# Kernel tuning notes

Hardware: AMD Instinct MI355X
Metric: run time of the kernel (lower is better)

## Reference

```python
import jax, jax.numpy as jnp
import numpy as np

N_NODES = 50000
N_EDGES = 800000
F_IN = 64
HID = 256
N_GRAPHS = 128
N_OUT = 24


def _sage_conv(x, src, dst, deg_inv, wl, bl, wr):
    # PyG SAGEConv (aggr='mean'): out = lin_l(mean_{j in N(i)} x_j) + lin_r(x_i)
    agg = jax.ops.segment_sum(x[src], dst, num_segments=x.shape[0]) * deg_inv
    return agg @ wl.T + bl + x @ wr.T


def setup_inputs() -> dict:
    key = jax.random.key(0)
    ks = jax.random.split(key, 16)
    x = jax.random.normal(ks[0], (N_NODES, F_IN), dtype=jnp.float32)
    edge_index = jax.random.randint(ks[1], (2, N_EDGES), 0, N_NODES, dtype=jnp.int64)
    batch = jnp.sort(jax.random.randint(ks[2], (N_NODES,), 0, N_GRAPHS, dtype=jnp.int64))

    def lin(k, fan_out, fan_in):
        bound = 1.0 / np.sqrt(fan_in)
        return jax.random.uniform(k, (fan_out, fan_in), jnp.float32, -bound, bound)

    inp = {
        'x': x, 'edge_index': edge_index, 'batch': batch,
        'w1l': lin(ks[3], HID, F_IN), 'b1': jnp.zeros((HID,), jnp.float32), 'w1r': lin(ks[4], HID, F_IN),
        'w2l': lin(ks[5], HID, HID), 'b2': jnp.zeros((HID,), jnp.float32), 'w2r': lin(ks[6], HID, HID),
        'w3l': lin(ks[7], HID, HID), 'b3': jnp.zeros((HID,), jnp.float32), 'w3r': lin(ks[8], HID, HID),
        'lin1_w': lin(ks[9], HID // 2, HID), 'lin1_b': jnp.zeros((HID // 2,), jnp.float32),
        'lin2_w': lin(ks[10], N_OUT, HID // 2), 'lin2_b': jnp.zeros((N_OUT,), jnp.float32),
    }
    return inp


def reference(x, edge_index, batch, w1l, b1, w1r, w2l, b2, w2r, w3l, b3, w3r,
              lin1_w, lin1_b, lin2_w, lin2_b):
    src, dst = edge_index[0], edge_index[1]
    deg = jax.ops.segment_sum(jnp.ones((src.shape[0],), jnp.float32), dst, num_segments=x.shape[0])
    deg_inv = (1.0 / jnp.maximum(deg, 1.0))[:, None]  # [N,1]

    h = jax.nn.relu(_sage_conv(x, src, dst, deg_inv, w1l, b1, w1r))
    h = jax.nn.relu(_sage_conv(h, src, dst, deg_inv, w2l, b2, w2r))
    h = jax.nn.relu(_sage_conv(h, src, dst, deg_inv, w3l, b3, w3r))

    # global mean pool over graphs
    pooled_sum = jax.ops.segment_sum(h, batch, num_segments=N_GRAPHS)
    counts = jax.ops.segment_sum(jnp.ones((h.shape[0],), jnp.float32), batch, num_segments=N_GRAPHS)
    pooled = pooled_sum / jnp.maximum(counts, 1.0)[:, None]

    g = jax.nn.relu(pooled @ lin1_w.T + lin1_b)
    return g @ lin2_w.T + lin2_b
```

## Files before the change

### kernel.cpp

```cpp
#include <hip/hip_runtime.h>

#define N_NODES 50000
#define M_PAD   50048
#define N_EDGES 800000
#define F_IN 64
#define HID 256
#define N_GRAPHS 128
#define N_OUT 24

typedef unsigned short ushort_t;
typedef __attribute__((ext_vector_type(8))) unsigned short us8;
typedef __attribute__((ext_vector_type(8))) __bf16 bf16x8;
typedef __attribute__((ext_vector_type(4))) float f32x4;

#define SLICE_US ((size_t)M_PAD * 32)

__device__ __forceinline__ unsigned short f2bf(float f) {
  unsigned u = __builtin_bit_cast(unsigned, f);
  return (unsigned short)((u + 0x7fffu + ((u >> 16) & 1u)) >> 16);
}
__device__ __forceinline__ float bf2f(unsigned short h) {
  return __builtin_bit_cast(float, (unsigned)h << 16);
}

__device__ __forceinline__ f32x4 mfma_bf16(us8 a, us8 b, f32x4 c) {
  return __builtin_amdgcn_mfma_f32_16x16x32_bf16(
      __builtin_bit_cast(bf16x8, a), __builtin_bit_cast(bf16x8, b), c, 0, 0, 0);
}

__device__ __forceinline__ void gload16(const ushort_t* g, ushort_t* l) {
  __builtin_amdgcn_global_load_lds(
      (const __attribute__((address_space(1))) void*)g,
      (__attribute__((address_space(3))) void*)l, 16, 0, 0);
}


__global__ void k_hist(const int* __restrict__ dst, int* __restrict__ deg_priv,
                       int* __restrict__ rank) {
  int e = blockIdx.x * 256 + threadIdx.x;
  if (e < N_EDGES) {
    int c = blockIdx.x & 7;
    rank[e] = atomicAdd(&deg_priv[c * N_NODES + dst[e]], 1);
  }
}

__global__ void k_gofs(const int* __restrict__ batch, int* __restrict__ gofs) {
  int t = threadIdx.x;
  if (t > N_GRAPHS) return;
  int lo = 0, hi = N_NODES;
  while (lo < hi) {
    int mid = (lo + hi) >> 1;
    if (batch[mid] < t) lo = mid + 1;
    else hi = mid;
  }
  gofs[t] = lo;
}

__global__ __launch_bounds__(1024) void k_scan1(int* __restrict__ deg_priv,
                                                int* __restrict__ deg,
                                                int* __restrict__ rowptr,
                                                int* __restrict__ partial) {
  __shared__ int s[1024];
  int t = threadIdx.x;
  int idx = blockIdx.x * 1024 + t;
  int v = 0;
  if (idx < N_NODES) {
    int run = 0;
#pragma unroll
    for (int c = 0; c < 8; ++c) {
      int dv = deg_priv[c * N_NODES + idx];
      deg_priv[c * N_NODES + idx] = run;
      run += dv;
    }
    deg[idx] = run;
    v = run;
  }
  s[t] = v;
  __syncthreads();
  for (int off = 1; off < 1024; off <<= 1) {
    int a = (t >= off) ? s[t - off] : 0;
    __syncthreads();
    s[t] += a;
    __syncthreads();
  }
  if (idx < N_NODES) rowptr[idx] = s[t] - v;
  if (t == 1023) partial[blockIdx.x] = s[1023];
}

__global__ void k_scan2(int* __restrict__ partial, int* __restrict__ rowptr) {
  __shared__ int s[64];
  int t = threadIdx.x;
  const int NB = (N_NODES + 1023) / 1024;
  int v = (t < NB) ? partial[t] : 0;
  s[t] = v;
  __syncthreads();
  for (int off = 1; off < 64; off <<= 1) {
    int a = (t >= off) ? s[t - off] : 0;
    __syncthreads();
    s[t] += a;
    __syncthreads();
  }
  if (t < NB) partial[t] = s[t] - v;
  if (t == NB - 1) rowptr[N_NODES] = s[t];
}

__global__ __launch_bounds__(1024) void k_scan3(const int* __restrict__ deg,
                                                const int* __restrict__ partial,
                                                int* __restrict__ rowptr,
                                                float* __restrict__ deg_inv) {
  int idx = blockIdx.x * 1024 + threadIdx.x;
  if (idx < N_NODES) {
    rowptr[idx] += partial[blockIdx.x];
    deg_inv[idx] = 1.0f / fmaxf((float)deg[idx], 1.0f);
  }
}

__global__ void k_place(const int* __restrict__ src, const int* __restrict__ dst,
                        const int* __restrict__ rowptr, const int* __restrict__ deg_priv,
                        const int* __restrict__ rank, int* __restrict__ esrc) {
  int e = blockIdx.x * 256 + threadIdx.x;
  if (e < N_EDGES) {
    int c = blockIdx.x & 7;
    int d = dst[e];
    esrc[rowptr[d] + deg_priv[c * N_NODES + d] + rank[e]] = src[e];
  }
}


__global__ void k_prep_x(const float* __restrict__ x, ushort_t* __restrict__ xio) {
  int g = blockIdx.x * 256 + threadIdx.x;
  if (g >= N_NODES * 8) return;
  int row = g >> 3, kb = g & 7;
  const float* p = x + (size_t)row * F_IN + kb * 8;
  us8 H, L;
#pragma unroll
  for (int i = 0; i < 8; ++i) {
    float f = p[i];
    unsigned short hi = f2bf(f);
    H[i] = hi;
    L[i] = f2bf(f - bf2f(hi));
  }
  size_t ob = (size_t)row * 128 + (size_t)((kb ^ (row & 7)) << 3);
  *(us8*)&xio[ob] = H;
  *(us8*)&xio[ob + 64] = L;
}

__global__ void k_prep_w(const float* __restrict__ w1lp, const float* __restrict__ w1rp,
                         const float* __restrict__ w2lp, const float* __restrict__ w2rp,
                         const float* __restrict__ w3lp, const float* __restrict__ w3rp,
                         ushort_t* __restrict__ wf1, ushort_t* __restrict__ wf2,
                         ushort_t* __restrict__ wf3) {
  int layer = blockIdx.z, side = blockIdx.y;
  const int Kg = (layer == 0) ? 8 : 32;
  const int qcs = Kg >> 2;
  int g = blockIdx.x * 256 + threadIdx.x;
  if (g >= 256 * Kg) return;
  const float* src = (layer == 0) ? (side ? w1rp : w1lp)
                   : (layer == 1) ? (side ? w2rp : w2lp)
                                  : (side ? w3rp : w3lp);
  ushort_t* dstf = (layer == 0) ? wf1 : (layer == 1) ? wf2 : wf3;
  int row = g / Kg, gb = g % Kg;
  const float* p = src + (size_t)row * (Kg * 8) + gb * 8;
  us8 H, L;
#pragma unroll
  for (int i = 0; i < 8; ++i) {
    float f = p[i];
    unsigned short hi = f2bf(f);
    H[i] = hi;
    L[i] = f2bf(f - bf2f(hi));
  }
  int nb2 = side * 16 + (row >> 4);
  int lane = (row & 15) + ((gb & 3) << 4);
  size_t base = ((size_t)(nb2 * qcs + (gb >> 2)) * 2) * 512 + lane * 8;
  *(us8*)&dstf[base] = H;
  *(us8*)&dstf[base + 512] = L;
}


__global__ __launch_bounds__(256) void k_agg64s(const float* __restrict__ x,
                                                const int* __restrict__ rowptr,
                                                const int* __restrict__ esrc,
                                                const float* __restrict__ deg_inv,
                                                ushort_t* __restrict__ oio) {
  int node = blockIdx.x * 4 + (threadIdx.x >> 6);
  if (node >= N_NODES) return;
  int lane = threadIdx.x & 63;
  int e0 = rowptr[node], e1 = rowptr[node + 1];
  float acc = 0.f;
  int e = e0;
  for (; e + 4 <= e1; e += 4) {
    int s0 = esrc[e], s1 = esrc[e + 1], s2 = esrc[e + 2], s3 = esrc[e + 3];
    float v0 = x[(size_t)s0 * F_IN + lane];
    float v1 = x[(size_t)s1 * F_IN + lane];
    float v2 = x[(size_t)s2 * F_IN + lane];
    float v3 = x[(size_t)s3 * F_IN + lane];
    acc += v0 + v1 + v2 + v3;
  }
  for (; e < e1; ++e) acc += x[(size_t)esrc[e] * F_IN + lane];
  acc *= deg_inv[node];
  unsigned short hi = f2bf(acc);
  unsigned short lo = f2bf(acc - bf2f(hi));
  size_t rb = (size_t)node * 128;
  int slot = ((lane >> 3) ^ (node & 7)) << 3;
  oio[rb + slot + (lane & 7)] = hi;
  oio[rb + 64 + slot + (lane & 7)] = lo;
}

__global__ __launch_bounds__(256) void k_agg256s(const ushort_t* __restrict__ hio,
                                                 const int* __restrict__ rowptr,
                                                 const int* __restrict__ esrc,
                                                 const float* __restrict__ deg_inv,
                                                 ushort_t* __restrict__ oio) {
  int c = blockIdx.x & 7;
  const ushort_t* hs = hio + (size_t)c * SLICE_US;
  ushort_t* os = oio + (size_t)c * SLICE_US;
  int q = threadIdx.x & 3;
  int ns = threadIdx.x >> 2;
  for (int base = (blockIdx.x >> 3) * 64; base < N_NODES; base += 16384) {
    int node = base + ns;
    if (node >= N_NODES) continue;
    int e0 = rowptr[node], e1 = rowptr[node + 1];
    float a[8] = {0.f, 0.f, 0.f, 0.f, 0.f, 0.f, 0.f, 0.f};
    int e = e0;
#pragma unroll 1
    for (; e + 4 <= e1; e += 4) {
      int s0 = esrc[e], s1 = esrc[e + 1], s2 = esrc[e + 2], s3 = esrc[e + 3];
      us8 v0 = *(const us8*)&hs[(size_t)s0 * 32 + ((q ^ (s0 & 3)) << 3)];
      us8 v1 = *(const us8*)&hs[(size_t)s1 * 32 + ((q ^ (s1 & 3)) << 3)];
      us8 v2 = *(const us8*)&hs[(size_t)s2 * 32 + ((q ^ (s2 & 3)) << 3)];
      us8 v3 = *(const us8*)&hs[(size_t)s3 * 32 + ((q ^ (s3 & 3)) << 3)];
#pragma unroll
      for (int i = 0; i < 8; ++i)
        a[i] += (bf2f(v0[i]) + bf2f(v1[i])) + (bf2f(v2[i]) + bf2f(v3[i]));
    }
    for (; e < e1; ++e) {
      int s = esrc[e];
      us8 v = *(const us8*)&hs[(size_t)s * 32 + ((q ^ (s & 3)) << 3)];
#pragma unroll
      for (int i = 0; i < 8; ++i) a[i] += bf2f(v[i]);
    }
    float di = deg_inv[node];
    us8 H;
#pragma unroll
    for (int i = 0; i < 8; ++i) H[i] = f2bf(a[i] * di);
    __builtin_nontemporal_store(
        H, (us8*)&os[(size_t)node * 32 + ((q ^ (node & 3)) << 3)]);
  }
}


template <int SA>
__global__ __launch_bounds__(256, SA ? 2 : 3) void k_gemm_mfma(
    const ushort_t* __restrict__ A1, int k1g, const ushort_t* __restrict__ w1f,
    const ushort_t* __restrict__ A2, int k2g, const ushort_t* __restrict__ w2f,
    const float* __restrict__ bias, ushort_t* __restrict__ oio,
    float* __restrict__ ofp, int mode) {
  __shared__ __align__(16) ushort_t ldsA[2][SA ? 8192 : 4096];

  int t = threadIdx.x;
  int wv = t >> 6, lane = t & 63;
  int fr = lane & 15, kq = lane >> 4;
  int bm = blockIdx.x;
  int rowA0 = bm * 64;

  f32x4 acc[4][4];
#pragma unroll
  for (int m = 0; m < 4; ++m)
#pragma unroll
    for (int n = 0; n < 4; ++n) acc[m][n] = (f32x4)0.f;

  const int ns1 = k1g >> 3, ns2 = k2g >> 3, ns = ns1 + ns2;
  const int lj = lane & 7, lr8 = lane >> 3;

  auto stage = [&](int buf, int s) {
    bool p2 = s >= ns1;
    const ushort_t* A = p2 ? A2 : A1;
    int Kg = p2 ? k2g : k1g;
    int sl = p2 ? (s - ns1) : s;
#pragma unroll
    for (int i = 0; i < 2; ++i) {
      int row = wv * 16 + i * 8 + lr8;
      int R = rowA0 + row;
      int lo = (wv * 16 + i * 8) * 64;
      if (SA) {
        size_t offA = ((size_t)R * (Kg * 2) + sl * 8 + lj) * 8;
        gload16(A + offA, &ldsA[buf][lo]);
        gload16(A + offA + (size_t)Kg * 8, &ldsA[buf][4096 + lo]);
      } else {
        size_t offA = (size_t)(sl * 2 + ((lj >> 2) ^ ((R >> 2) & 1))) * SLICE_US +
                      (size_t)R * 32 + (size_t)((lj & 3) << 3);
        gload16(A + offA, &ldsA[buf][lo]);
      }
    }
  };

  stage(0, 0);
  __syncthreads();
  int cur = 0;

  for (int s = 0; s < ns; ++s) {
    bool p2 = s >= ns1;
    const ushort_t* Wf = p2 ? w2f : w1f;
    int sl = p2 ? (s - ns1) : s;
    int qcs = (p2 ? k2g : k1g) >> 2;

    us8 bh[2][4], bl[2][4];
#pragma unroll
    for (int kc = 0; kc < 2; ++kc)
#pragma unroll
      for (int n = 0; n < 4; ++n) {
        size_t base = ((size_t)((wv * 4 + n) * qcs + sl * 2 + kc) * 2) * 512 + lane * 8;
        bh[kc][n] = *(const us8*)&Wf[base];
        bl[kc][n] = *(const us8*)&Wf[base + 512];
      }

    if (s + 1 < ns) stage(cur ^ 1, s + 1);

#pragma unroll
    for (int kc = 0; kc < 2; ++kc) {
      int kg = kc * 4 + kq;
      int swk = (kg ^ (fr & 7)) << 3;
      us8 ah[4], al[4];
#pragma unroll
      for (int m = 0; m < 4; ++m) {
        int off = ((m * 16 + fr) << 6) + swk;
        ah[m] = *(const us8*)&ldsA[cur][off];
        if (SA) al[m] = *(const us8*)&ldsA[cur][4096 + off];
      }
#pragma unroll
      for (int m = 0; m < 4; ++m)
#pragma unroll
        for (int n = 0; n < 4; ++n)
          acc[m][n] = mfma_bf16(ah[m], bh[kc][n], acc[m][n]);
#pragma unroll
      for (int m = 0; m < 4; ++m)
#pragma unroll
        for (int n = 0; n < 4; ++n)
          acc[m][n] = mfma_bf16(ah[m], bl[kc][n], acc[m][n]);
      if (SA) {
#pragma unroll
        for (int m = 0; m < 4; ++m)
#pragma unroll
          for (int n = 0; n < 4; ++n)
            acc[m][n] = mfma_bf16(al[m], bh[kc][n], acc[m][n]);
      }
    }
    __syncthreads();
    cur ^= 1;
  }

#pragma unroll
  for (int n = 0; n < 4; ++n) {
    int colg = wv * 64 + n * 16 + fr;
    float bv = bias[colg];
#pragma unroll
    for (int m = 0; m < 4; ++m) {
      f32x4 v = acc[m][n];
      int rowb = bm * 64 + m * 16 + kq * 4;
#pragma unroll
      for (int r = 0; r < 4; ++r) {
        int rowg = rowb + r;
        if (rowg < N_NODES) {
          float h = fmaxf(v[r] + bv, 0.f);
          if (mode == 0) {
            int gi = colg >> 3;
            size_t addr = (size_t)(gi >> 2) * SLICE_US + (size_t)rowg * 32 +
                          (size_t)((((gi & 3) ^ (rowg & 3)) << 3) + (colg & 7));
            oio[addr] = f2bf(h);
          } else {
            ofp[(size_t)rowg * HID + colg] = h;
          }
        }
      }
    }
  }
}


__global__ __launch_bounds__(256) void k_pool(const float* __restrict__ h,
                                              const int* __restrict__ gofs,
                                              float* __restrict__ pooled) {
  int g = blockIdx.y, c = blockIdx.x;
  int r0 = gofs[g], r1 = gofs[g + 1];
  int rg = threadIdx.x >> 6, lane = threadIdx.x & 63;
  float ax = 0.f, ay = 0.f, az = 0.f, aw = 0.f;
  for (int r = r0 + c * 4 + rg; r < r1; r += 64) {
    float4 v = *(const float4*)&h[(size_t)r * HID + lane * 4];
    ax += v.x; ay += v.y; az += v.z; aw += v.w;
  }
  __shared__ float4 sm[4][64];
  sm[rg][lane] = make_float4(ax, ay, az, aw);
  __syncthreads();
  if (rg == 0) {
    float4 s0 = sm[0][lane], s1 = sm[1][lane], s2 = sm[2][lane], s3 = sm[3][lane];
    float* p = &pooled[g * HID + lane * 4];
    atomicAdd(p + 0, s0.x + s1.x + s2.x + s3.x);
    atomicAdd(p + 1, s0.y + s1.y + s2.y + s3.y);
    atomicAdd(p + 2, s0.z + s1.z + s2.z + s3.z);
    atomicAdd(p + 3, s0.w + s1.w + s2.w + s3.w);
  }
}


__global__ __launch_bounds__(128) void k_head(const float* __restrict__ pooled,
                                              const int* __restrict__ gofs,
                                              const float* __restrict__ w1,
                                              const float* __restrict__ b1,
                                              const float* __restrict__ w2,
                                              const float* __restrict__ b2,
                                              float* __restrict__ out) {
  __shared__ float p[HID];
  __shared__ float g1[HID / 2];
  int g = blockIdx.x, t = threadIdx.x;
  float inv = 1.f / fmaxf((float)(gofs[g + 1] - gofs[g]), 1.f);
  p[t] = pooled[g * HID + t] * inv;
  p[t + 128] = pooled[g * HID + 128 + t] * inv;
  __syncthreads();
  float s = b1[t];
#pragma unroll 4
  for (int k = 0; k < HID; ++k) s = fmaf(p[k], w1[t * HID + k], s);
  g1[t] = fmaxf(s, 0.f);
  __syncthreads();
  if (t < N_OUT) {
    float s2 = b2[t];
#pragma unroll 4
    for (int k = 0; k < HID / 2; ++k) s2 = fmaf(g1[k], w2[t * (HID / 2) + k], s2);
    out[g * N_OUT + t] = s2;
  }
}


extern "C" void kernel_launch(void* const* d_in, const int* in_sizes, int n_in,
                              void* d_out, int out_size, void* d_ws, size_t ws_size,
                              hipStream_t stream) {
  const float* x      = (const float*)d_in[0];
  const int*   ei     = (const int*)d_in[1];
  const int*   batch  = (const int*)d_in[2];
  const float* w1lw   = (const float*)d_in[3];
  const float* b1     = (const float*)d_in[4];
  const float* w1rw   = (const float*)d_in[5];
  const float* w2lw   = (const float*)d_in[6];
  const float* b2     = (const float*)d_in[7];
  const float* w2rw   = (const float*)d_in[8];
  const float* w3lw   = (const float*)d_in[9];
  const float* b3     = (const float*)d_in[10];
  const float* w3rw   = (const float*)d_in[11];
  const float* lin1_w = (const float*)d_in[12];
  const float* lin1_b = (const float*)d_in[13];
  const float* lin2_w = (const float*)d_in[14];
  const float* lin2_b = (const float*)d_in[15];
  float* out = (float*)d_out;

  const int* srcIdx = ei;
  const int* dstIdx = ei + N_EDGES;

  size_t off = 0;
  auto carve = [&](size_t bytes) {
    size_t r = off;
    off += (bytes + 255) & ~(size_t)255;
    return r;
  };
  char* ws = (char*)d_ws;
  int*      deg_priv = (int*)(ws + carve((size_t)8 * N_NODES * 4));
  int*      deg      = (int*)(ws + carve((size_t)N_NODES * 4));
  int*      rank     = (int*)(ws + carve((size_t)N_EDGES * 4));
  int*      rowptr   = (int*)(ws + carve((size_t)(N_NODES + 1) * 4));
  float*    deg_inv  = (float*)(ws + carve((size_t)N_NODES * 4));
  int*      esrc     = (int*)(ws + carve((size_t)N_EDGES * 4));
  int*      partial  = (int*)(ws + carve(64 * 4));
  int*      gofs     = (int*)(ws + carve((N_GRAPHS + 1) * 4));
  ushort_t* xio      = (ushort_t*)(ws + carve((size_t)M_PAD * 128 * 2));
  ushort_t* agg1     = (ushort_t*)(ws + carve((size_t)M_PAD * 128 * 2));
  ushort_t* agg      = (ushort_t*)(ws + carve((size_t)M_PAD * 256 * 2));
  char*     h1blk    = ws + carve((size_t)M_PAD * HID * 4);
  ushort_t* h1       = (ushort_t*)h1blk;
  float*    h3       = (float*)h1blk;
  ushort_t* h2       = (ushort_t*)(ws + carve((size_t)M_PAD * 256 * 2));
  ushort_t* wf1      = (ushort_t*)(ws + carve((size_t)2 * 32768 * 2));
  ushort_t* wf2      = (ushort_t*)(ws + carve((size_t)2 * 131072 * 2));
  ushort_t* wf3      = (ushort_t*)(ws + carve((size_t)2 * 131072 * 2));
  float*    pooled   = (float*)(ws + carve((size_t)N_GRAPHS * HID * 4));
  (void)ws_size; (void)n_in; (void)in_sizes; (void)out_size;

  hipMemsetAsync(deg_priv, 0, (size_t)8 * N_NODES * 4, stream);
  hipMemsetAsync(pooled, 0, (size_t)N_GRAPHS * HID * 4, stream);

  const int EB = (N_EDGES + 255) / 256;
  const int SB = (N_NODES + 1023) / 1024;

  k_hist<<<EB, 256, 0, stream>>>(dstIdx, deg_priv, rank);
  k_gofs<<<1, 256, 0, stream>>>(batch, gofs);
  k_scan1<<<SB, 1024, 0, stream>>>(deg_priv, deg, rowptr, partial);
  k_scan2<<<1, 64, 0, stream>>>(partial, rowptr);
  k_scan3<<<SB, 1024, 0, stream>>>(deg, partial, rowptr, deg_inv);
  k_place<<<EB, 256, 0, stream>>>(srcIdx, dstIdx, rowptr, deg_priv, rank, esrc);

  k_prep_x<<<(N_NODES * 8 + 255) / 256, 256, 0, stream>>>(x, xio);
  k_prep_w<<<dim3(32, 2, 3), 256, 0, stream>>>(w1lw, w1rw, w2lw, w2rw, w3lw, w3rw,
                                               wf1, wf2, wf3);

  const int GB = M_PAD / 64;
  const int AB = N_NODES / 4;
  const int AGB = 2048;

  k_agg64s<<<AB, 256, 0, stream>>>(x, rowptr, esrc, deg_inv, agg1);
  k_gemm_mfma<1><<<GB, 256, 0, stream>>>(agg1, 8, wf1,
                                         xio, 8, wf1 + 32768,
                                         b1, h1, nullptr, 0);
  k_agg256s<<<AGB, 256, 0, stream>>>(h1, rowptr, esrc, deg_inv, agg);
  k_gemm_mfma<0><<<GB, 256, 0, stream>>>(agg, 32, wf2,
                                         h1, 32, wf2 + 131072,
                                         b2, h2, nullptr, 0);
  k_agg256s<<<AGB, 256, 0, stream>>>(h2, rowptr, esrc, deg_inv, agg);
  k_gemm_mfma<0><<<GB, 256, 0, stream>>>(agg, 32, wf3,
                                         h2, 32, wf3 + 131072,
                                         b3, nullptr, h3, 1);

  k_pool<<<dim3(16, N_GRAPHS), 256, 0, stream>>>(h3, gofs, pooled);
  k_head<<<N_GRAPHS, 128, 0, stream>>>(pooled, gofs, lin1_w, lin1_b, lin2_w, lin2_b, out);
}
```

Measured before the change: 381.9 us.

## Load whole K panel into LDS per operand instead of double-buffered k-steps

The GEMM kernel drops its double-buffered per-k-step A staging. For each of the two input operands (aggregated and self features) it now loads the full K-width tile into LDS at once, synchronises, then runs all k-substeps from LDS. This removes a barrier per k-step and the rolling prefetch, but no longer overlaps global loads with MFMA work. It also enlarges LDS for the non-SA path and lowers its occupancy hint from 3 to 2 blocks. The layout and swizzle are rewritten and now hardcode per-operand K sizes (SA assumes 128 columns, non-SA assumes 256).

```diff
diff --git a/kernel.cpp b/kernel.cpp
--- a/kernel.cpp
+++ b/kernel.cpp
@@ -250,12 +250,14 @@
 
 
 template <int SA>
-__global__ __launch_bounds__(256, SA ? 2 : 3) void k_gemm_mfma(
+__global__ __launch_bounds__(256, 2) void k_gemm_mfma(
     const ushort_t* __restrict__ A1, int k1g, const ushort_t* __restrict__ w1f,
     const ushort_t* __restrict__ A2, int k2g, const ushort_t* __restrict__ w2f,
     const float* __restrict__ bias, ushort_t* __restrict__ oio,
     float* __restrict__ ofp, int mode) {
-  __shared__ __align__(16) ushort_t ldsA[2][SA ? 8192 : 4096];
+  __shared__ __align__(16) ushort_t ldsA[SA ? 8192 : 16384];
+  const int PG = SA ? 2 : 4;
+  const int NSUB = SA ? 1 : 4;
 
   int t = threadIdx.x;
   int wv = t >> 6, lane = t & 63;
@@ -269,84 +271,79 @@
 #pragma unroll
     for (int n = 0; n < 4; ++n) acc[m][n] = (f32x4)0.f;
 
-  const int ns1 = k1g >> 3, ns2 = k2g >> 3, ns = ns1 + ns2;
   const int lj = lane & 7, lr8 = lane >> 3;
 
-  auto stage = [&](int buf, int s) {
-    bool p2 = s >= ns1;
-    const ushort_t* A = p2 ? A2 : A1;
-    int Kg = p2 ? k2g : k1g;
-    int sl = p2 ? (s - ns1) : s;
-#pragma unroll
-    for (int i = 0; i < 2; ++i) {
-      int row = wv * 16 + i * 8 + lr8;
-      int R = rowA0 + row;
-      int lo = (wv * 16 + i * 8) * 64;
-      if (SA) {
-        size_t offA = ((size_t)R * (Kg * 2) + sl * 8 + lj) * 8;
-        gload16(A + offA, &ldsA[buf][lo]);
-        gload16(A + offA + (size_t)Kg * 8, &ldsA[buf][4096 + lo]);
-      } else {
-        size_t offA = (size_t)(sl * 2 + ((lj >> 2) ^ ((R >> 2) & 1))) * SLICE_US +
-                      (size_t)R * 32 + (size_t)((lj & 3) << 3);
-        gload16(A + offA, &ldsA[buf][lo]);
+  for (int p = 0; p < 2; ++p) {
+    const ushort_t* A = p ? A2 : A1;
+    if (SA) {
+#pragma unroll
+      for (int i = 0; i < 4; ++i) {
+        int rowgrp = wv * 2 + (i & 1);
+        int posgrp = i >> 1;
+        int R = rowA0 + rowgrp * 8 + lr8;
+        size_t src = (size_t)R * 128 + (size_t)(posgrp * 64 + lj * 8);
+        gload16(A + src, &ldsA[(rowgrp * 2 + posgrp) * 512]);
       }
-    }
-  };
-
-  stage(0, 0);
-  __syncthreads();
-  int cur = 0;
-
-  for (int s = 0; s < ns; ++s) {
-    bool p2 = s >= ns1;
-    const ushort_t* Wf = p2 ? w2f : w1f;
-    int sl = p2 ? (s - ns1) : s;
-    int qcs = (p2 ? k2g : k1g) >> 2;
-
-    us8 bh[2][4], bl[2][4];
-#pragma unroll
-    for (int kc = 0; kc < 2; ++kc)
-#pragma unroll
-      for (int n = 0; n < 4; ++n) {
-        size_t base = ((size_t)((wv * 4 + n) * qcs + sl * 2 + kc) * 2) * 512 + lane * 8;
-        bh[kc][n] = *(const us8*)&Wf[base];
-        bl[kc][n] = *(const us8*)&Wf[base + 512];
-      }
-
-    if (s + 1 < ns) stage(cur ^ 1, s + 1);
-
-#pragma unroll
-    for (int kc = 0; kc < 2; ++kc) {
-      int kg = kc * 4 + kq;
-      int swk = (kg ^ (fr & 7)) << 3;
-      us8 ah[4], al[4];
-#pragma unroll
-      for (int m = 0; m < 4; ++m) {
-        int off = ((m * 16 + fr) << 6) + swk;
-        ah[m] = *(const us8*)&ldsA[cur][off];
-        if (SA) al[m] = *(const us8*)&ldsA[cur][4096 + off];
-      }
-#pragma unroll
-      for (int m = 0; m < 4; ++m)
-#pragma unroll
-        for (int n = 0; n < 4; ++n)
-          acc[m][n] = mfma_bf16(ah[m], bh[kc][n], acc[m][n]);
-#pragma unroll
-      for (int m = 0; m < 4; ++m)
-#pragma unroll
-        for (int n = 0; n < 4; ++n)
-          acc[m][n] = mfma_bf16(ah[m], bl[kc][n], acc[m][n]);
-      if (SA) {
-#pragma unroll
-        for (int m = 0; m < 4; ++m)
-#pragma unroll
-          for (int n = 0; n < 4; ++n)
-            acc[m][n] = mfma_bf16(al[m], bh[kc][n], acc[m][n]);
+    } else {
+#pragma unroll
+      for (int i = 0; i < 8; ++i) {
+        int rowgrp = wv * 2 + (i & 1);
+        int posgrp = i >> 1;
+        int R = rowA0 + rowgrp * 8 + lr8;
+        int G = posgrp * 8 + (lj ^ (R & 7));
+        size_t src = (size_t)(G >> 2) * SLICE_US + (size_t)R * 32 +
+                     (size_t)(((G & 3) ^ (R & 3)) << 3);
+        gload16(A + src, &ldsA[(rowgrp * PG + posgrp) * 512]);
       }
     }
     __syncthreads();
-    cur ^= 1;
+
+    const ushort_t* Wf = p ? w2f : w1f;
+    const int qcs = (p ? k2g : k1g) >> 2;
+
+#pragma unroll
+    for (int ss = 0; ss < NSUB; ++ss) {
+      us8 bh[2][4], bl[2][4];
+#pragma unroll
+      for (int kc = 0; kc < 2; ++kc)
+#pragma unroll
+        for (int n = 0; n < 4; ++n) {
+          size_t base =
+              ((size_t)((wv * 4 + n) * qcs + ss * 2 + kc)) * 1024 + lane * 8;
+          bh[kc][n] = *(const us8*)&Wf[base];
+          bl[kc][n] = *(const us8*)&Wf[base + 512];
+        }
+#pragma unroll
+      for (int kc = 0; kc < 2; ++kc) {
+        int swz = (kc * 4 + kq) ^ (fr & 7);
+        us8 ah[4], al[4];
+#pragma unroll
+        for (int m = 0; m < 4; ++m) {
+          int idx = (((m * 2 + (fr >> 3)) * PG + ss) << 9) + ((fr & 7) << 6) +
+                    (swz << 3);
+          ah[m] = *(const us8*)&ldsA[idx];
+          if (SA) al[m] = *(const us8*)&ldsA[idx + 512];
+        }
+#pragma unroll
+        for (int m = 0; m < 4; ++m)
+#pragma unroll
+          for (int n = 0; n < 4; ++n)
+            acc[m][n] = mfma_bf16(ah[m], bh[kc][n], acc[m][n]);
+#pragma unroll
+        for (int m = 0; m < 4; ++m)
+#pragma unroll
+          for (int n = 0; n < 4; ++n)
+            acc[m][n] = mfma_bf16(ah[m], bl[kc][n], acc[m][n]);
+        if (SA) {
+#pragma unroll
+          for (int m = 0; m < 4; ++m)
+#pragma unroll
+            for (int n = 0; n < 4; ++n)
+              acc[m][n] = mfma_bf16(al[m], bh[kc][n], acc[m][n]);
+        }
+      }
+    }
+    __syncthreads();
   }
 
 #pragma unroll
```

After: 410.4 us. 7.5% more time.
